# Kernel tuning notes

Hardware: AMD Instinct MI355X
Metric: run time of the kernel (lower is better)

The kernel has to match this reference:

```python
import jax, jax.numpy as jnp
import numpy as np

IN_DIM, OUT_DIM, K, NUM = 512, 512, 3, 16
BATCH = 256


def setup_inputs() -> dict:
    key = jax.random.key(0)
    k1, k2 = jax.random.split(key, 2)
    x = jax.random.normal(k1, (BATCH, IN_DIM), dtype=jnp.float32)
    # uniform grid on [-1,1] extended by K knots each side (extend_grid)
    h = 2.0 / NUM
    g1d = jnp.arange(-K, NUM + K + 1, dtype=jnp.float32) * h - 1.0  # (NUM+1+2K,)
    grid = jnp.tile(g1d[None, :], (IN_DIM, 1))  # (in_dim, 24)
    coef = jax.random.normal(k2, (IN_DIM, OUT_DIM, NUM + K), dtype=jnp.float32) * 0.1
    scale_sp = jnp.ones((IN_DIM, OUT_DIM), jnp.float32) * (1.0 / np.sqrt(IN_DIM).astype(np.float32))
    mask = jnp.ones((IN_DIM, OUT_DIM), jnp.float32)
    return {"x": x, "grid": grid, "coef": coef, "scale_sp": scale_sp, "mask": mask}


def b_spline_basis(x, grid, k):
    # x: (B, I); grid: (I, G).  Cox-de Boor recursion, vectorized.
    xg = x[:, :, None]          # (B, I, 1)
    g = grid[None, :, :]        # (1, I, G)
    B = ((xg >= g[:, :, :-1]) & (xg < g[:, :, 1:])).astype(x.dtype)  # order-0
    for kk in range(1, k + 1):
        B = ((xg - g[:, :, :-(kk + 1)]) / (g[:, :, kk:-1] - g[:, :, :-(kk + 1)]) * B[:, :, :-1]
             + (g[:, :, kk + 1:] - xg) / (g[:, :, kk + 1:] - g[:, :, 1:-kk]) * B[:, :, 1:])
    return B  # (B, I, NUM + K)


def reference(x, grid, coef, scale_sp, mask):
    base = jax.nn.silu(x)                              # (B, I) base_fun branch
    Bmat = b_spline_basis(x, grid, K)                  # (B, I, NUM+K)
    y = jnp.einsum('big,iog->bio', Bmat, coef)         # coef2curve -> (B, I, O)
    y = (base[:, :, None] + scale_sp[None, :, :] * y) * mask[None, :, :]
    return jnp.sum(y, axis=1)                          # (B, O)
```

## Files before the change

kernel.cpp:

```cpp
#include <hip/hip_runtime.h>

#define IN_DIM   512
#define OUT_DIM  512
#define KDEG     3
#define BATCH    256
#define NB       19
#define NG       23
#define KAUG     20
#define KTOT     (IN_DIM * KAUG)

typedef short  bf16x8 __attribute__((ext_vector_type(8)));
typedef float  f32x4  __attribute__((ext_vector_type(4)));

__device__ __forceinline__ unsigned short f2bf(float f) {
    union { float f; unsigned int u; } v; v.f = f;
    unsigned int r = (v.u + 0x7FFF + ((v.u >> 16) & 1)) >> 16;
    return (unsigned short)r;
}

__device__ __forceinline__ float bf2f(unsigned short h) {
    union { unsigned int u; float f; } v;
    v.u = ((unsigned int)h) << 16;
    return v.f;
}

__global__ void build_A(const float* __restrict__ X,
                        const float* __restrict__ G,
                        unsigned short* __restrict__ A) {
    int t = blockIdx.x * blockDim.x + threadIdx.x;
    if (t >= BATCH * IN_DIM) return;
    int b = t / IN_DIM;
    int i = t - b * IN_DIM;

    float x = X[t];

    float gr[NG];
    const float* g = G + i * NG;
#pragma unroll
    for (int j = 0; j < NG; j++) gr[j] = g[j];

    float B[NG - 1];
#pragma unroll
    for (int j = 0; j < NG - 1; j++)
        B[j] = (x >= gr[j] && x < gr[j + 1]) ? 1.0f : 0.0f;

#pragma unroll
    for (int kk = 1; kk <= KDEG; kk++) {
#pragma unroll
        for (int j = 0; j < NG - 1 - kk; j++) {
            float d1 = gr[j + kk] - gr[j];
            float d2 = gr[j + kk + 1] - gr[j + 1];
            B[j] = (x - gr[j]) / d1 * B[j] +
                   (gr[j + kk + 1] - x) / d2 * B[j + 1];
        }
    }

    unsigned short v[KAUG];
#pragma unroll
    for (int j = 0; j < NB; j++) v[j] = f2bf(B[j]);
    v[NB] = f2bf(x / (1.0f + __expf(-x)));

    unsigned int* dst = (unsigned int*)(A + (size_t)b * KTOT + i * KAUG);
    const unsigned int* src = (const unsigned int*)v;
#pragma unroll
    for (int d = 0; d < KAUG / 2; d++) dst[d] = src[d];
}

#define BN     32
#define SPLITS 32
#define ICH    16
#define KCH    (ICH * KAUG)
#define LDS_K  (KCH + 8)

__global__ __launch_bounds__(512, 4) void gemm_fused(
        const unsigned short* __restrict__ A,
        const float* __restrict__ coef,
        const float* __restrict__ scale_sp,
        const float* __restrict__ mask,
        unsigned short* __restrict__ P) {
    __shared__ __align__(16) unsigned short Bs[BN * LDS_K];

    int tid = threadIdx.x;
    int o0 = blockIdx.x * BN;
    int i0 = blockIdx.z * ICH;
    int kbase = blockIdx.z * KCH;

    {
        int o  = tid & 31;
        int di = tid >> 5;
        int io = (i0 + di) * OUT_DIM + (o0 + o);
        float m  = mask[io];
        float sm = scale_sp[io] * m;
        const float* c = coef + (size_t)io * NB;

        __align__(8) unsigned short v[KAUG];
#pragma unroll
        for (int g = 0; g < NB; g++) v[g] = f2bf(c[g] * sm);
        v[NB] = f2bf(m);

        unsigned long long* dst =
            (unsigned long long*)((char*)Bs + (size_t)o * (LDS_K * 2) + di * (KAUG * 2));
        const unsigned long long* src = (const unsigned long long*)v;
#pragma unroll
        for (int d = 0; d < 5; d++) dst[d] = src[d];
    }
    __syncthreads();

    int lane = tid & 63;
    int w    = tid >> 6;
    int quad = lane >> 4;
    int lr   = lane & 15;

    f32x4 acc[2][2];
#pragma unroll
    for (int i = 0; i < 2; i++)
#pragma unroll
        for (int j = 0; j < 2; j++) acc[i][j] = (f32x4)0.0f;

    const unsigned short* a0 = A + (size_t)(w * 32 + lr)      * KTOT + kbase + quad * 8;
    const unsigned short* a1 = A + (size_t)(w * 32 + 16 + lr) * KTOT + kbase + quad * 8;
    const unsigned short* b0 = &Bs[(size_t)lr        * LDS_K + quad * 8];
    const unsigned short* b1 = &Bs[(size_t)(16 + lr) * LDS_K + quad * 8];

#pragma unroll
    for (int kk = 0; kk < KCH; kk += 32) {
        bf16x8 af0 = *(const bf16x8*)(a0 + kk);
        bf16x8 af1 = *(const bf16x8*)(a1 + kk);
        bf16x8 bf0 = *(const bf16x8*)(b0 + kk);
        bf16x8 bf1 = *(const bf16x8*)(b1 + kk);
        acc[0][0] = __builtin_amdgcn_mfma_f32_16x16x32_bf16(af0, bf0, acc[0][0], 0, 0, 0);
        acc[0][1] = __builtin_amdgcn_mfma_f32_16x16x32_bf16(af0, bf1, acc[0][1], 0, 0, 0);
        acc[1][0] = __builtin_amdgcn_mfma_f32_16x16x32_bf16(af1, bf0, acc[1][0], 0, 0, 0);
        acc[1][1] = __builtin_amdgcn_mfma_f32_16x16x32_bf16(af1, bf1, acc[1][1], 0, 0, 0);
    }

    unsigned short* Pz = P + (size_t)blockIdx.z * BATCH * OUT_DIM;
#pragma unroll
    for (int mt = 0; mt < 2; mt++) {
#pragma unroll
        for (int nt = 0; nt < 2; nt++) {
            int col = o0 + nt * 16 + lr;
            int rb  = w * 32 + mt * 16 + quad * 4;
#pragma unroll
            for (int r = 0; r < 4; r++)
                Pz[(size_t)(rb + r) * OUT_DIM + col] = f2bf(acc[mt][nt][r]);
        }
    }
}

__global__ __launch_bounds__(256) void reduce_out(const unsigned short* __restrict__ P,
                                                  float* __restrict__ out) {
    int e8 = blockIdx.x * blockDim.x + threadIdx.x;
    float s[8] = {};
#pragma unroll
    for (int zz = 0; zz < SPLITS; zz++) {
        bf16x8 v = *(const bf16x8*)(P + (size_t)zz * BATCH * OUT_DIM + (size_t)e8 * 8);
#pragma unroll
        for (int j = 0; j < 8; j++)
            s[j] += bf2f((unsigned short)v[j]);
    }
    f32x4* o4 = (f32x4*)(out + (size_t)e8 * 8);
    o4[0] = *(f32x4*)&s[0];
    o4[1] = *(f32x4*)&s[4];
}

extern "C" void kernel_launch(void* const* d_in, const int* in_sizes, int n_in,
                              void* d_out, int out_size, void* d_ws, size_t ws_size,
                              hipStream_t stream) {
    const float* x        = (const float*)d_in[0];
    const float* grid     = (const float*)d_in[1];
    const float* coef     = (const float*)d_in[2];
    const float* scale_sp = (const float*)d_in[3];
    const float* mask     = (const float*)d_in[4];
    float* out = (float*)d_out;

    unsigned short* A = (unsigned short*)d_ws;
    unsigned short* P = (unsigned short*)((char*)d_ws + (size_t)BATCH * KTOT * 2);

    build_A<<<dim3((BATCH * IN_DIM + 255) / 256), dim3(256), 0, stream>>>(x, grid, A);

    gemm_fused<<<dim3(OUT_DIM / BN, 1, SPLITS), dim3(512), 0, stream>>>(
        A, coef, scale_sp, mask, P);

    reduce_out<<<dim3(BATCH * OUT_DIM / 8 / 256), dim3(256), 0, stream>>>(P, out);
}
```

Before: 98.83 us.

## Coalesce coef loads via LDS staging, remap block order, halve reduce vector width

The GEMM kernel now stages each block's coef slab through shared memory with contiguous, coalesced loads, replacing the strided per-thread 19-float reads. It also flattens the grid to 1D and swizzles the block-to-(split, output tile) mapping. The basis builder replaces per-term divisions with precomputed reciprocals, and the reduce kernel uses 4-wide loads with twice as many threads. The cost is extra LDS (about 39KB of float staging), which may lower occupancy.

```diff
diff --git a/kernel.cpp b/kernel.cpp
--- a/kernel.cpp
+++ b/kernel.cpp
@@ -10,6 +10,7 @@
 #define KTOT     (IN_DIM * KAUG)
 
 typedef short  bf16x8 __attribute__((ext_vector_type(8)));
+typedef short  bf16x4 __attribute__((ext_vector_type(4)));
 typedef float  f32x4  __attribute__((ext_vector_type(4)));
 
 __device__ __forceinline__ unsigned short f2bf(float f) {
@@ -29,8 +30,8 @@
                         unsigned short* __restrict__ A) {
     int t = blockIdx.x * blockDim.x + threadIdx.x;
     if (t >= BATCH * IN_DIM) return;
-    int b = t / IN_DIM;
-    int i = t - b * IN_DIM;
+    int b = t >> 9;
+    int i = t & (IN_DIM - 1);
 
     float x = X[t];
 
@@ -46,13 +47,14 @@
 
 #pragma unroll
     for (int kk = 1; kk <= KDEG; kk++) {
-#pragma unroll
-        for (int j = 0; j < NG - 1 - kk; j++) {
-            float d1 = gr[j + kk] - gr[j];
-            float d2 = gr[j + kk + 1] - gr[j + 1];
-            B[j] = (x - gr[j]) / d1 * B[j] +
-                   (gr[j + kk + 1] - x) / d2 * B[j + 1];
-        }
+        float inv[NG];
+#pragma unroll
+        for (int j = 0; j < NG - kk; j++)
+            inv[j] = 1.0f / (gr[j + kk] - gr[j]);
+#pragma unroll
+        for (int j = 0; j < NG - 1 - kk; j++)
+            B[j] = (x - gr[j]) * inv[j] * B[j] +
+                   (gr[j + kk + 1] - x) * inv[j + 1] * B[j + 1];
     }
 
     unsigned short v[KAUG];
@@ -71,6 +73,7 @@
 #define ICH    16
 #define KCH    (ICH * KAUG)
 #define LDS_K  (KCH + 8)
+#define SLAB   (BN * NB)
 
 __global__ __launch_bounds__(512, 4) void gemm_fused(
         const unsigned short* __restrict__ A,
@@ -79,23 +82,39 @@
         const float* __restrict__ mask,
         unsigned short* __restrict__ P) {
     __shared__ __align__(16) unsigned short Bs[BN * LDS_K];
+    __shared__ __align__(16) float stag[ICH][SLAB];
 
     int tid = threadIdx.x;
-    int o0 = blockIdx.x * BN;
-    int i0 = blockIdx.z * ICH;
-    int kbase = blockIdx.z * KCH;
+
+    int linear = blockIdx.x;
+    int z  = ((linear & 7) << 2) + (linear >> 7);
+    int ob = (linear >> 3) & 15;
+    int o0 = ob * BN;
+    int i0 = z * ICH;
+    int kbase = z * KCH;
+
+    int o  = tid & 31;
+    int di = tid >> 5;
+    int io = (i0 + di) * OUT_DIM + (o0 + o);
+    float m  = mask[io];
+    float sm = scale_sp[io] * m;
 
     {
-        int o  = tid & 31;
-        int di = tid >> 5;
-        int io = (i0 + di) * OUT_DIM + (o0 + o);
-        float m  = mask[io];
-        float sm = scale_sp[io] * m;
-        const float* c = coef + (size_t)io * NB;
-
+        const float* cbase = coef + ((size_t)i0 * OUT_DIM + o0) * NB;
+#pragma unroll
+        for (int r = 0; r < ICH; ++r) {
+            const float* run = cbase + (size_t)r * OUT_DIM * NB;
+            stag[r][tid] = run[tid];
+            if (tid < SLAB - 512) stag[r][512 + tid] = run[512 + tid];
+        }
+    }
+    __syncthreads();
+
+    {
+        const float* cs = &stag[di][o * NB];
         __align__(8) unsigned short v[KAUG];
 #pragma unroll
-        for (int g = 0; g < NB; g++) v[g] = f2bf(c[g] * sm);
+        for (int g2 = 0; g2 < NB; g2++) v[g2] = f2bf(cs[g2] * sm);
         v[NB] = f2bf(m);
 
         unsigned long long* dst =
@@ -134,7 +153,7 @@
         acc[1][1] = __builtin_amdgcn_mfma_f32_16x16x32_bf16(af1, bf1, acc[1][1], 0, 0, 0);
     }
 
-    unsigned short* Pz = P + (size_t)blockIdx.z * BATCH * OUT_DIM;
+    unsigned short* Pz = P + (size_t)z * BATCH * OUT_DIM;
 #pragma unroll
     for (int mt = 0; mt < 2; mt++) {
 #pragma unroll
@@ -150,18 +169,18 @@
 
 __global__ __launch_bounds__(256) void reduce_out(const unsigned short* __restrict__ P,
                                                   float* __restrict__ out) {
-    int e8 = blockIdx.x * blockDim.x + threadIdx.x;
-    float s[8] = {};
+    int e4 = blockIdx.x * blockDim.x + threadIdx.x;
+    float s0 = 0.f, s1 = 0.f, s2 = 0.f, s3 = 0.f;
 #pragma unroll
     for (int zz = 0; zz < SPLITS; zz++) {
-        bf16x8 v = *(const bf16x8*)(P + (size_t)zz * BATCH * OUT_DIM + (size_t)e8 * 8);
-#pragma unroll
-        for (int j = 0; j < 8; j++)
-            s[j] += bf2f((unsigned short)v[j]);
-    }
-    f32x4* o4 = (f32x4*)(out + (size_t)e8 * 8);
-    o4[0] = *(f32x4*)&s[0];
-    o4[1] = *(f32x4*)&s[4];
+        bf16x4 v = *(const bf16x4*)(P + (size_t)zz * BATCH * OUT_DIM + (size_t)e4 * 4);
+        s0 += bf2f((unsigned short)v[0]);
+        s1 += bf2f((unsigned short)v[1]);
+        s2 += bf2f((unsigned short)v[2]);
+        s3 += bf2f((unsigned short)v[3]);
+    }
+    f32x4 r = { s0, s1, s2, s3 };
+    *(f32x4*)(out + (size_t)e4 * 4) = r;
 }
 
 extern "C" void kernel_launch(void* const* d_in, const int* in_sizes, int n_in,
@@ -179,8 +198,8 @@
 
     build_A<<<dim3((BATCH * IN_DIM + 255) / 256), dim3(256), 0, stream>>>(x, grid, A);
 
-    gemm_fused<<<dim3(OUT_DIM / BN, 1, SPLITS), dim3(512), 0, stream>>>(
+    gemm_fused<<<dim3(OUT_DIM / BN * SPLITS), dim3(512), 0, stream>>>(
         A, coef, scale_sp, mask, P);
 
-    reduce_out<<<dim3(BATCH * OUT_DIM / 8 / 256), dim3(256), 0, stream>>>(P, out);
-}
+    reduce_out<<<dim3(BATCH * OUT_DIM / 4 / 256), dim3(256), 0, stream>>>(P, out);
+}
```

Result: slower. 101.7 us (+2.9%).
